# Kernel optimization log

Hardware: AMD Instinct MI355X
Metric: run time of the kernel (lower is better)

The kernel has to match this reference:

```python
import jax, jax.numpy as jnp
import numpy as np

B, T, D, UNITS = 64, 1024, 512, 1024

def setup_inputs() -> dict:
    key = jax.random.key(0)
    ks = jax.random.split(key, 8)
    s = lambda fan_in: 1.0 / np.sqrt(fan_in)
    return {
        "features": jax.random.normal(ks[0], (B, T, D), dtype=jnp.float32),
        "hidden": jax.random.normal(ks[1], (B, D), dtype=jnp.float32),
        "W1_w": jax.random.normal(ks[2], (D, UNITS), dtype=jnp.float32) * s(D),
        "W1_b": jnp.zeros((UNITS,), dtype=jnp.float32),
        "W2_w": jax.random.normal(ks[3], (D, UNITS), dtype=jnp.float32) * s(D),
        "W2_b": jnp.zeros((UNITS,), dtype=jnp.float32),
        "V_w": jax.random.normal(ks[4], (UNITS, 1), dtype=jnp.float32) * s(UNITS),
        "V_b": jnp.zeros((1,), dtype=jnp.float32),
    }

def reference(features, hidden, W1_w, W1_b, W2_w, W2_b, V_w, V_b):
    # features: [B,T,D], hidden: [B,D]
    proj_f = jnp.einsum('btd,du->btu', features, W1_w) + W1_b          # [B,T,U]
    proj_h = (hidden @ W2_w + W2_b)[:, None, :]                        # [B,1,U]
    score = jnp.tanh(proj_f + proj_h)                                  # [B,T,U]
    logits = jnp.einsum('btu,uo->bto', score, V_w) + V_b               # [B,T,1]
    attention_weights = jax.nn.softmax(logits, axis=1)                 # [B,T,1]
    context_vector = jnp.sum(attention_weights * features, axis=1)     # [B,D]
    return context_vector, attention_weights
```

## Files before the change

kernel.cpp:

```cpp
#include <hip/hip_runtime.h>
#include <math.h>

#define B_ 64
#define T_ 1024
#define D_ 512
#define U_ 1024

typedef __bf16 bf16x8 __attribute__((ext_vector_type(8)));
typedef float f32x16 __attribute__((ext_vector_type(16)));
typedef unsigned int u32;

__device__ __forceinline__ float fast_tanh(float x) {
    float ax = fabsf(x);
    float e = __expf(2.0f * ax);
    float r = 1.0f - __fdividef(2.0f, e + 1.0f);
    return copysignf(r, x);
}

__device__ __forceinline__ u32 f2bf_pk(float lo, float hi) {
    u32 a = __float_as_uint(lo) + 0x8000u;
    u32 b = __float_as_uint(hi) + 0x8000u;
    return (a >> 16) | (b & 0xffff0000u);
}

__global__ __launch_bounds__(256) void prep_kernel(
    const float* __restrict__ W1, const float* __restrict__ hidden,
    const float* __restrict__ W2, const float* __restrict__ W2b,
    const float* __restrict__ W1b,
    unsigned short* __restrict__ W1F, float* __restrict__ ph) {
    if (blockIdx.x < 256) {
        const int gid  = blockIdx.x * 256 + threadIdx.x;
        const int lane = gid & 63;
        const int frag = gid >> 6;
        const int ks = frag & 1;
        const int kt = (frag >> 1) & 15;
        const int ut = frag >> 5;
        const int u  = ut * 32 + (lane & 31);
        const int k0 = kt * 32 + ks * 16 + (lane >> 5) * 8;
        float f[8];
#pragma unroll
        for (int j = 0; j < 8; ++j) f[j] = W1[(size_t)(k0 + j) * U_ + u];
        uint4 w;
        w.x = f2bf_pk(f[0], f[1]);
        w.y = f2bf_pk(f[2], f[3]);
        w.z = f2bf_pk(f[4], f[5]);
        w.w = f2bf_pk(f[6], f[7]);
        *(uint4*)&W1F[(size_t)gid * 8] = w;
    } else {
        const int bx = blockIdx.x - 256;
        const int u  = (bx & 3) * 256 + threadIdx.x;
        const int b  = bx >> 2;
        const float* h = hidden + b * D_;
        float acc = 0.f;
#pragma unroll 8
        for (int d = 0; d < D_; ++d) acc = fmaf(h[d], W2[(size_t)d * U_ + u], acc);
        ph[b * U_ + u] = acc + W2b[u] + W1b[u];
    }
}

__global__ __launch_bounds__(512, 4) void logits_mfma_kernel(
    const float* __restrict__ feat,
    const unsigned short* __restrict__ W1F,
    const float* __restrict__ ph,
    const float* __restrict__ Vw,
    float* __restrict__ lpart) {
    __shared__ __align__(16) char As[65536];

    const int tid  = threadIdx.x;
    const int gx   = blockIdx.x;
    const int uh   = gx & 1;
    const int tt   = gx >> 1;
    const int b    = blockIdx.y;
    const int t0   = tt * 64;
    const int lane = tid & 63;
    const int widx = tid >> 6;
    const int l31 = lane & 31, g = lane >> 5;
    const int u0  = uh * 512 + widx * 64;

    {
        const int r  = tid >> 3;
        const int s0 = tid & 7;
        const float* src = feat + ((size_t)(b * T_ + t0 + r)) * D_;
        const int xr = (r >> 2) & 3;
#pragma unroll
        for (int i = 0; i < 8; ++i) {
            const int s = s0 + 8 * i;
            const float4 v0 = *(const float4*)(src + s * 8);
            const float4 v1 = *(const float4*)(src + s * 8 + 4);
            uint4 w;
            w.x = f2bf_pk(v0.x, v0.y);
            w.y = f2bf_pk(v0.z, v0.w);
            w.z = f2bf_pk(v1.x, v1.y);
            w.w = f2bf_pk(v1.z, v1.w);
            const int panel = s >> 2, q = s & 3;
            *(uint4*)&As[panel * 4096 + r * 64 + (q ^ xr) * 16] = w;
        }
    }
    __syncthreads();

    const char* bfbase = (const char*)W1F + (size_t)(u0 >> 5) * 32768 + lane * 16;
    auto loadB = [&](bf16x8* dst, int kt) {
#pragma unroll
        for (int nt = 0; nt < 2; ++nt)
#pragma unroll
            for (int ks = 0; ks < 2; ++ks)
                dst[nt * 2 + ks] =
                    *(const bf16x8*)(bfbase + nt * 32768 + (kt * 2 + ks) * 1024);
    };

    f32x16 acc[2][2];
#pragma unroll
    for (int mt = 0; mt < 2; ++mt)
#pragma unroll
        for (int nt = 0; nt < 2; ++nt) acc[mt][nt] = (f32x16)(0.f);

    auto computeStep = [&](int kt, const bf16x8* bfr) {
        bf16x8 af[2][2];
#pragma unroll
        for (int ks = 0; ks < 2; ++ks)
#pragma unroll
            for (int mt = 0; mt < 2; ++mt) {
                const int rr = mt * 32 + l31;
                const int q  = (2 * ks + g) ^ ((rr >> 2) & 3);
                af[ks][mt] = *(const bf16x8*)&As[kt * 4096 + rr * 64 + q * 16];
            }
#pragma unroll
        for (int ks = 0; ks < 2; ++ks)
#pragma unroll
            for (int mt = 0; mt < 2; ++mt)
#pragma unroll
                for (int nt = 0; nt < 2; ++nt)
                    acc[mt][nt] = __builtin_amdgcn_mfma_f32_32x32x16_bf16(
                        af[ks][mt], bfr[nt * 2 + ks], acc[mt][nt], 0, 0, 0);
    };

    bf16x8 b0[4], b1[4];
    loadB(b0, 0);
    for (int kt = 0; kt < 16; kt += 2) {
        if (kt + 1 < 16) loadB(b1, kt + 1);
        computeStep(kt, b0);
        if (kt + 2 < 16) loadB(b0, kt + 2);
        computeStep(kt + 1, b1);
    }

    float lp[2][16];
#pragma unroll
    for (int mt = 0; mt < 2; ++mt)
#pragma unroll
        for (int r = 0; r < 16; ++r) lp[mt][r] = 0.f;

#pragma unroll
    for (int nt = 0; nt < 2; ++nt) {
        const int u = u0 + nt * 32 + l31;
        const float phv = ph[b * U_ + u];
        const float vw  = Vw[u];
#pragma unroll
        for (int mt = 0; mt < 2; ++mt)
#pragma unroll
            for (int r = 0; r < 16; ++r)
                lp[mt][r] = fmaf(vw, fast_tanh(acc[mt][nt][r] + phv), lp[mt][r]);
    }
#pragma unroll
    for (int mt = 0; mt < 2; ++mt)
#pragma unroll
        for (int r = 0; r < 16; ++r) {
            float v = lp[mt][r];
            v += __shfl_xor(v, 1);
            v += __shfl_xor(v, 2);
            v += __shfl_xor(v, 4);
            v += __shfl_xor(v, 8);
            v += __shfl_xor(v, 16);
            lp[mt][r] = v;
        }
    __syncthreads();
    float* scr = (float*)&As[0];
    if (l31 == 0) {
#pragma unroll
        for (int mt = 0; mt < 2; ++mt)
#pragma unroll
            for (int r = 0; r < 16; ++r) {
                const int row = mt * 32 + (r & 3) + 8 * (r >> 2) + 4 * g;
                scr[row * 8 + widx] = lp[mt][r];
            }
    }
    __syncthreads();
    if (tid < 64) {
        float s = 0.f;
#pragma unroll
        for (int x = 0; x < 8; ++x) s += scr[tid * 8 + x];
        lpart[((size_t)uh * B_ + b) * T_ + t0 + tid] = s;
    }
}

__global__ __launch_bounds__(256) void ctx_kernel(
    const float* __restrict__ feat, const float* __restrict__ lpart,
    float* __restrict__ attn, float* __restrict__ part) {
    const int b   = blockIdx.y;
    const int seg = blockIdx.x;
    const int tid = threadIdx.x;
    __shared__ float wls[1024];
    __shared__ float redm[4];
    __shared__ float reds[4];

    float v[4];
    float mx = -3.4e38f;
#pragma unroll
    for (int j = 0; j < 4; ++j) {
        const int x = b * T_ + tid + 256 * j;
        v[j] = lpart[x] + lpart[B_ * T_ + x];
        mx = fmaxf(mx, v[j]);
    }
#pragma unroll
    for (int off = 32; off > 0; off >>= 1) mx = fmaxf(mx, __shfl_xor(mx, off));
    if ((tid & 63) == 0) redm[tid >> 6] = mx;
    __syncthreads();
    mx = fmaxf(fmaxf(redm[0], redm[1]), fmaxf(redm[2], redm[3]));
    float s = 0.f;
#pragma unroll
    for (int j = 0; j < 4; ++j) {
        v[j] = __expf(v[j] - mx);
        s += v[j];
    }
#pragma unroll
    for (int off = 32; off > 0; off >>= 1) s += __shfl_xor(s, off);
    if ((tid & 63) == 0) reds[tid >> 6] = s;
    __syncthreads();
    s = reds[0] + reds[1] + reds[2] + reds[3];
    const float inv = 1.0f / s;
#pragma unroll
    for (int j = 0; j < 4; ++j) wls[tid + 256 * j] = v[j] * inv;
    __syncthreads();

    if (tid < 128) attn[b * T_ + seg * 128 + tid] = wls[seg * 128 + tid];

    const int d4 = (tid & 127) * 4;
    const int h  = tid >> 7;
    const int t0 = seg * 128 + h * 64;
    const float* fb = feat + ((size_t)b * T_ + t0) * D_ + d4;
    const float* wb = &wls[t0];
    float4 acc = {0.f, 0.f, 0.f, 0.f};
#pragma unroll 4
    for (int t = 0; t < 64; ++t) {
        const float w  = wb[t];
        const float4 f = *(const float4*)&fb[(size_t)t * D_];
        acc.x = fmaf(w, f.x, acc.x);
        acc.y = fmaf(w, f.y, acc.y);
        acc.z = fmaf(w, f.z, acc.z);
        acc.w = fmaf(w, f.w, acc.w);
    }
    *(float4*)&part[((size_t)(b * 16 + seg * 2 + h)) * D_ + d4] = acc;
}

__global__ __launch_bounds__(256) void context_reduce_kernel(
    const float* __restrict__ part, float* __restrict__ ctx) {
    const int i = blockIdx.x * 256 + threadIdx.x;
    const int b = i >> 9;
    const int d = i & (D_ - 1);
    float s = 0.f;
#pragma unroll
    for (int g = 0; g < 16; ++g) s += part[((size_t)(b * 16 + g)) * D_ + d];
    ctx[i] = s;
}

extern "C" void kernel_launch(void* const* d_in, const int* in_sizes, int n_in,
                              void* d_out, int out_size, void* d_ws, size_t ws_size,
                              hipStream_t stream) {
    const float* feat   = (const float*)d_in[0];
    const float* hidden = (const float*)d_in[1];
    const float* W1w    = (const float*)d_in[2];
    const float* W1b    = (const float*)d_in[3];
    const float* W2w    = (const float*)d_in[4];
    const float* W2b    = (const float*)d_in[5];
    const float* Vw     = (const float*)d_in[6];

    float* out_ctx  = (float*)d_out;
    float* out_attn = out_ctx + B_ * D_;

    unsigned short* W1F = (unsigned short*)d_ws;
    float* ph     = (float*)(W1F + (size_t)U_ * D_);
    float* lpart  = ph + B_ * U_;
    float* part   = lpart + 2 * B_ * T_;

    prep_kernel<<<512, 256, 0, stream>>>(W1w, hidden, W2w, W2b, W1b, W1F, ph);
    logits_mfma_kernel<<<dim3(32, B_), 512, 0, stream>>>(feat, W1F, ph, Vw, lpart);
    ctx_kernel<<<dim3(8, B_), 256, 0, stream>>>(feat, lpart, out_attn, part);
    context_reduce_kernel<<<B_ * D_ / 256, 256, 0, stream>>>(part, out_ctx);
}
```

Measured before the change: 331.8 us.

## Process both U halves per block to reuse staged features, atomic ctx reduce

Each logits block now loops over both 512-column halves of U, reusing the bf16 feature tile already staged in LDS. This halves the feature loads and conversions and the block count. Per-wave partial logits are written straight to a [B,T,16] buffer, which drops the LDS cross-wave reduction and its barriers. The ctx kernel sums those 16 partials, uses 512 threads, and accumulates context with atomicAdd into an output zeroed in prep, so the separate reduce kernel goes away. MFMA sections are also wrapped in s_setprio. The costs are a longer serial per-block loop, less grid parallelism, and atomic contention.

```diff
diff --git a/kernel.cpp b/kernel.cpp
--- a/kernel.cpp
+++ b/kernel.cpp
@@ -27,7 +27,8 @@
     const float* __restrict__ W1, const float* __restrict__ hidden,
     const float* __restrict__ W2, const float* __restrict__ W2b,
     const float* __restrict__ W1b,
-    unsigned short* __restrict__ W1F, float* __restrict__ ph) {
+    unsigned short* __restrict__ W1F, float* __restrict__ ph,
+    float* __restrict__ ctx0) {
     if (blockIdx.x < 256) {
         const int gid  = blockIdx.x * 256 + threadIdx.x;
         const int lane = gid & 63;
@@ -48,6 +49,8 @@
         *(uint4*)&W1F[(size_t)gid * 8] = w;
     } else {
         const int bx = blockIdx.x - 256;
+        const int zi = bx * 256 + (int)threadIdx.x;
+        if (zi < B_ * D_) ctx0[zi] = 0.f;
         const int u  = (bx & 3) * 256 + threadIdx.x;
         const int b  = bx >> 2;
         const float* h = hidden + b * D_;
@@ -67,15 +70,12 @@
     __shared__ __align__(16) char As[65536];
 
     const int tid  = threadIdx.x;
-    const int gx   = blockIdx.x;
-    const int uh   = gx & 1;
-    const int tt   = gx >> 1;
+    const int tt   = blockIdx.x;
     const int b    = blockIdx.y;
     const int t0   = tt * 64;
     const int lane = tid & 63;
     const int widx = tid >> 6;
     const int l31 = lane & 31, g = lane >> 5;
-    const int u0  = uh * 512 + widx * 64;
 
     {
         const int r  = tid >> 3;
@@ -98,21 +98,20 @@
     }
     __syncthreads();
 
-    const char* bfbase = (const char*)W1F + (size_t)(u0 >> 5) * 32768 + lane * 16;
-    auto loadB = [&](bf16x8* dst, int kt) {
+    const char* bb0 = (const char*)W1F + (size_t)(widx * 2) * 32768 + lane * 16;
+    const char* bb1 = bb0 + (size_t)16 * 32768;
+
+    f32x16 acc[2][2];
+    bf16x8 b0[4], b1[4];
+
+    auto loadB = [&](const char* bb, bf16x8* dst, int kt) {
 #pragma unroll
         for (int nt = 0; nt < 2; ++nt)
 #pragma unroll
             for (int ks = 0; ks < 2; ++ks)
                 dst[nt * 2 + ks] =
-                    *(const bf16x8*)(bfbase + nt * 32768 + (kt * 2 + ks) * 1024);
+                    *(const bf16x8*)(bb + nt * 32768 + (kt * 2 + ks) * 1024);
     };
-
-    f32x16 acc[2][2];
-#pragma unroll
-    for (int mt = 0; mt < 2; ++mt)
-#pragma unroll
-        for (int nt = 0; nt < 2; ++nt) acc[mt][nt] = (f32x16)(0.f);
 
     auto computeStep = [&](int kt, const bf16x8* bfr) {
         bf16x8 af[2][2];
@@ -124,6 +123,7 @@
                 const int q  = (2 * ks + g) ^ ((rr >> 2) & 3);
                 af[ks][mt] = *(const bf16x8*)&As[kt * 4096 + rr * 64 + q * 16];
             }
+        __builtin_amdgcn_s_setprio(1);
 #pragma unroll
         for (int ks = 0; ks < 2; ++ks)
 #pragma unroll
@@ -132,92 +132,98 @@
                 for (int nt = 0; nt < 2; ++nt)
                     acc[mt][nt] = __builtin_amdgcn_mfma_f32_32x32x16_bf16(
                         af[ks][mt], bfr[nt * 2 + ks], acc[mt][nt], 0, 0, 0);
+        __builtin_amdgcn_s_setprio(0);
     };
 
-    bf16x8 b0[4], b1[4];
-    loadB(b0, 0);
-    for (int kt = 0; kt < 16; kt += 2) {
-        if (kt + 1 < 16) loadB(b1, kt + 1);
-        computeStep(kt, b0);
-        if (kt + 2 < 16) loadB(b0, kt + 2);
-        computeStep(kt + 1, b1);
-    }
-
-    float lp[2][16];
-#pragma unroll
-    for (int mt = 0; mt < 2; ++mt)
-#pragma unroll
-        for (int r = 0; r < 16; ++r) lp[mt][r] = 0.f;
-
-#pragma unroll
-    for (int nt = 0; nt < 2; ++nt) {
-        const int u = u0 + nt * 32 + l31;
-        const float phv = ph[b * U_ + u];
-        const float vw  = Vw[u];
+    loadB(bb0, b0, 0);
+#pragma unroll
+    for (int uh = 0; uh < 2; ++uh) {
+        const char* bb = uh ? bb1 : bb0;
 #pragma unroll
         for (int mt = 0; mt < 2; ++mt)
 #pragma unroll
-            for (int r = 0; r < 16; ++r)
-                lp[mt][r] = fmaf(vw, fast_tanh(acc[mt][nt][r] + phv), lp[mt][r]);
-    }
-#pragma unroll
-    for (int mt = 0; mt < 2; ++mt)
-#pragma unroll
-        for (int r = 0; r < 16; ++r) {
-            float v = lp[mt][r];
-            v += __shfl_xor(v, 1);
-            v += __shfl_xor(v, 2);
-            v += __shfl_xor(v, 4);
-            v += __shfl_xor(v, 8);
-            v += __shfl_xor(v, 16);
-            lp[mt][r] = v;
-        }
-    __syncthreads();
-    float* scr = (float*)&As[0];
-    if (l31 == 0) {
+            for (int nt = 0; nt < 2; ++nt) acc[mt][nt] = (f32x16)(0.f);
+
+        for (int kt = 0; kt < 16; kt += 2) {
+            loadB(bb, b1, kt + 1);
+            computeStep(kt, b0);
+            if (kt + 2 < 16) loadB(bb, b0, kt + 2);
+            computeStep(kt + 1, b1);
+        }
+        if (uh == 0) loadB(bb1, b0, 0);
+
+        float lp[2][16];
 #pragma unroll
         for (int mt = 0; mt < 2; ++mt)
 #pragma unroll
+            for (int r = 0; r < 16; ++r) lp[mt][r] = 0.f;
+
+#pragma unroll
+        for (int nt = 0; nt < 2; ++nt) {
+            const int u = uh * 512 + widx * 64 + nt * 32 + l31;
+            const float phv = ph[b * U_ + u];
+            const float vw  = Vw[u];
+#pragma unroll
+            for (int mt = 0; mt < 2; ++mt)
+#pragma unroll
+                for (int r = 0; r < 16; ++r)
+                    lp[mt][r] = fmaf(vw, fast_tanh(acc[mt][nt][r] + phv), lp[mt][r]);
+        }
+#pragma unroll
+        for (int mt = 0; mt < 2; ++mt)
+#pragma unroll
             for (int r = 0; r < 16; ++r) {
-                const int row = mt * 32 + (r & 3) + 8 * (r >> 2) + 4 * g;
-                scr[row * 8 + widx] = lp[mt][r];
+                float v = lp[mt][r];
+                v += __shfl_xor(v, 1);
+                v += __shfl_xor(v, 2);
+                v += __shfl_xor(v, 4);
+                v += __shfl_xor(v, 8);
+                v += __shfl_xor(v, 16);
+                lp[mt][r] = v;
             }
-    }
-    __syncthreads();
-    if (tid < 64) {
-        float s = 0.f;
-#pragma unroll
-        for (int x = 0; x < 8; ++x) s += scr[tid * 8 + x];
-        lpart[((size_t)uh * B_ + b) * T_ + t0 + tid] = s;
-    }
-}
-
-__global__ __launch_bounds__(256) void ctx_kernel(
+        if (l31 == 0) {
+#pragma unroll
+            for (int mt = 0; mt < 2; ++mt)
+#pragma unroll
+                for (int r = 0; r < 16; ++r) {
+                    const int row = mt * 32 + (r & 3) + 8 * (r >> 2) + 4 * g;
+                    lpart[((size_t)(b * T_ + t0 + row)) * 16 + uh * 8 + widx] =
+                        lp[mt][r];
+                }
+        }
+    }
+}
+
+__global__ __launch_bounds__(512) void ctx_kernel(
     const float* __restrict__ feat, const float* __restrict__ lpart,
-    float* __restrict__ attn, float* __restrict__ part) {
+    float* __restrict__ attn, float* __restrict__ ctx_out) {
     const int b   = blockIdx.y;
     const int seg = blockIdx.x;
     const int tid = threadIdx.x;
     __shared__ float wls[1024];
-    __shared__ float redm[4];
-    __shared__ float reds[4];
-
-    float v[4];
+    __shared__ float redm[8];
+    __shared__ float reds[8];
+
+    float v[2];
     float mx = -3.4e38f;
 #pragma unroll
-    for (int j = 0; j < 4; ++j) {
-        const int x = b * T_ + tid + 256 * j;
-        v[j] = lpart[x] + lpart[B_ * T_ + x];
+    for (int j = 0; j < 2; ++j) {
+        const float4* p =
+            (const float4*)&lpart[((size_t)(b * T_) + tid + 512 * j) * 16];
+        const float4 a = p[0], c = p[1], d = p[2], e = p[3];
+        v[j] = ((a.x + a.y) + (a.z + a.w)) + ((c.x + c.y) + (c.z + c.w)) +
+               ((d.x + d.y) + (d.z + d.w)) + ((e.x + e.y) + (e.z + e.w));
         mx = fmaxf(mx, v[j]);
     }
 #pragma unroll
     for (int off = 32; off > 0; off >>= 1) mx = fmaxf(mx, __shfl_xor(mx, off));
     if ((tid & 63) == 0) redm[tid >> 6] = mx;
     __syncthreads();
-    mx = fmaxf(fmaxf(redm[0], redm[1]), fmaxf(redm[2], redm[3]));
+    mx = fmaxf(fmaxf(fmaxf(redm[0], redm[1]), fmaxf(redm[2], redm[3])),
+               fmaxf(fmaxf(redm[4], redm[5]), fmaxf(redm[6], redm[7])));
     float s = 0.f;
 #pragma unroll
-    for (int j = 0; j < 4; ++j) {
+    for (int j = 0; j < 2; ++j) {
         v[j] = __expf(v[j] - mx);
         s += v[j];
     }
@@ -225,22 +231,23 @@
     for (int off = 32; off > 0; off >>= 1) s += __shfl_xor(s, off);
     if ((tid & 63) == 0) reds[tid >> 6] = s;
     __syncthreads();
-    s = reds[0] + reds[1] + reds[2] + reds[3];
+    s = ((reds[0] + reds[1]) + (reds[2] + reds[3])) +
+        ((reds[4] + reds[5]) + (reds[6] + reds[7]));
     const float inv = 1.0f / s;
-#pragma unroll
-    for (int j = 0; j < 4; ++j) wls[tid + 256 * j] = v[j] * inv;
+    wls[tid]       = v[0] * inv;
+    wls[tid + 512] = v[1] * inv;
     __syncthreads();
 
     if (tid < 128) attn[b * T_ + seg * 128 + tid] = wls[seg * 128 + tid];
 
+    const int q  = tid >> 7;
     const int d4 = (tid & 127) * 4;
-    const int h  = tid >> 7;
-    const int t0 = seg * 128 + h * 64;
-    const float* fb = feat + ((size_t)b * T_ + t0) * D_ + d4;
+    const int t0 = seg * 128 + q * 32;
+    const float* fb = feat + ((size_t)(b * T_ + t0)) * D_ + d4;
     const float* wb = &wls[t0];
     float4 acc = {0.f, 0.f, 0.f, 0.f};
 #pragma unroll 4
-    for (int t = 0; t < 64; ++t) {
+    for (int t = 0; t < 32; ++t) {
         const float w  = wb[t];
         const float4 f = *(const float4*)&fb[(size_t)t * D_];
         acc.x = fmaf(w, f.x, acc.x);
@@ -248,18 +255,11 @@
         acc.z = fmaf(w, f.z, acc.z);
         acc.w = fmaf(w, f.w, acc.w);
     }
-    *(float4*)&part[((size_t)(b * 16 + seg * 2 + h)) * D_ + d4] = acc;
-}
-
-__global__ __launch_bounds__(256) void context_reduce_kernel(
-    const float* __restrict__ part, float* __restrict__ ctx) {
-    const int i = blockIdx.x * 256 + threadIdx.x;
-    const int b = i >> 9;
-    const int d = i & (D_ - 1);
-    float s = 0.f;
-#pragma unroll
-    for (int g = 0; g < 16; ++g) s += part[((size_t)(b * 16 + g)) * D_ + d];
-    ctx[i] = s;
+    float* dst = ctx_out + b * D_ + d4;
+    atomicAdd(dst + 0, acc.x);
+    atomicAdd(dst + 1, acc.y);
+    atomicAdd(dst + 2, acc.z);
+    atomicAdd(dst + 3, acc.w);
 }
 
 extern "C" void kernel_launch(void* const* d_in, const int* in_sizes, int n_in,
@@ -279,10 +279,10 @@
     unsigned short* W1F = (unsigned short*)d_ws;
     float* ph     = (float*)(W1F + (size_t)U_ * D_);
     float* lpart  = ph + B_ * U_;
-    float* part   = lpart + 2 * B_ * T_;
-
-    prep_kernel<<<512, 256, 0, stream>>>(W1w, hidden, W2w, W2b, W1b, W1F, ph);
-    logits_mfma_kernel<<<dim3(32, B_), 512, 0, stream>>>(feat, W1F, ph, Vw, lpart);
-    ctx_kernel<<<dim3(8, B_), 256, 0, stream>>>(feat, lpart, out_attn, part);
-    context_reduce_kernel<<<B_ * D_ / 256, 256, 0, stream>>>(part, out_ctx);
-}
+
+    prep_kernel<<<512, 256, 0, stream>>>(W1w, hidden, W2w, W2b, W1b, W1F, ph,
+                                         out_ctx);
+    logits_mfma_kernel<<<dim3(16, B_), 512, 0, stream>>>(feat, W1F, ph, Vw,
+                                                         lpart);
+    ctx_kernel<<<dim3(8, B_), 512, 0, stream>>>(feat, lpart, out_attn, out_ctx);
+}
```

Result: slower. 403.1 us (+21.5%).
